# Performance work log

Hardware: AMD Instinct MI355X
Metric: run time of the kernel (lower is better)

The kernel has to match this reference:

```python
import jax, jax.numpy as jnp
import numpy as np

N = 50000
E_G = 600000
E_K = 500000
IN_FEATS = 64
H = 128
C = 2
# calculate_theta2(d=2): Bernstein polynomial coefficients (ascending powers)
THETAS_G = [[3.0, -3.0, 0.75], [0.0, 3.0, -1.5], [0.0, 0.0, 0.75]]
THETAS_K = [[1.0, 1.0, 1.0]] * 3


def _xavier(key, shape):
    fan_in, fan_out = shape[1], shape[0]
    lim = float(np.sqrt(6.0 / (fan_in + fan_out)))
    return jax.random.uniform(key, shape, jnp.float32, -lim, lim)


def setup_inputs() -> dict:
    key = jax.random.key(0)
    ks = jax.random.split(key, 32)
    inp = {
        "x": jax.random.normal(ks[0], (N, IN_FEATS), jnp.float32),
        "src_g": jax.random.randint(ks[1], (E_G,), 0, N, jnp.int32),
        "dst_g": jax.random.randint(ks[2], (E_G,), 0, N, jnp.int32),
        "src_k": jax.random.randint(ks[3], (E_K,), 0, N, jnp.int32),
        "dst_k": jax.random.randint(ks[4], (E_K,), 0, N, jnp.int32),
        # input MLP
        "W1": _xavier(ks[5], (H, IN_FEATS)), "b1": jnp.zeros((H,), jnp.float32),
        "W2": _xavier(ks[6], (H, H)), "b2": jnp.zeros((H,), jnp.float32),
        # 3 PolyConvs on main graph: learnable_diag [3,3,H], linear [3,H,H]+bias
        "diag_g": jax.random.uniform(ks[7], (3, 3, H), jnp.float32),
        "Wc_g": jnp.stack([_xavier(ks[8 + i], (H, H)) for i in range(3)]),
        "bc_g": jnp.zeros((3, H), jnp.float32),
        # 3 PolyConvs on knn graph
        "diag_k": jax.random.uniform(ks[11], (3, 3, H), jnp.float32),
        "Wc_k": jnp.stack([_xavier(ks[12 + i], (H, H)) for i in range(3)]),
        "bc_k": jnp.zeros((3, H), jnp.float32),
        # fusion linears (3H -> H)
        "W3": _xavier(ks[15], (H, 3 * H)), "b3": jnp.zeros((H,), jnp.float32),
        "Wk": _xavier(ks[16], (H, 3 * H)), "bk": jnp.zeros((H,), jnp.float32),
        # ComponentAttention: Linear(H,H)+Tanh+Linear(H,1,no bias)
        "Wa1": _xavier(ks[17], (H, H)), "ba1": jnp.zeros((H,), jnp.float32),
        "Wa2": _xavier(ks[18], (1, H)),
        # classifier
        "W4": _xavier(ks[19], (C, H)), "b4": jnp.zeros((C,), jnp.float32),
    }
    return inp


def _dinvsqrt(dst, n):
    deg = jax.ops.segment_sum(jnp.ones(dst.shape, jnp.float32), dst, num_segments=n)
    return jnp.clip(deg, 1.0, None) ** -0.5  # [N]


def _poly_conv(feat, src, dst, dinv, theta, diag, W, b, n):
    # h = linear(theta[0]*feat * diag[0]); then k-1 Laplacian hops
    h = jnp.dot((theta[0] * feat) * diag[0], W.T) + b
    for k in range(1, len(theta)):
        m = feat * dinv  # [N,H]
        agg = jax.ops.segment_sum(m[src], dst, num_segments=n)  # SpMM
        feat = feat - (agg * dinv) * diag[k]
        h = h + theta[k] * feat
    return h


def reference(x, src_g, dst_g, src_k, dst_k, W1, b1, W2, b2, diag_g, Wc_g, bc_g,
              diag_k, Wc_k, bc_k, W3, b3, Wk, bk, Wa1, ba1, Wa2, W4, b4):
    dinv_g = _dinvsqrt(dst_g, N)[:, None]
    dinv_k = _dinvsqrt(dst_k, N)[:, None]

    h = jax.nn.relu(jnp.dot(x, W1.T) + b1)
    h = jax.nn.relu(jnp.dot(h, W2.T) + b2)

    h_o = jnp.concatenate(
        [_poly_conv(h, src_g, dst_g, dinv_g, THETAS_G[i], diag_g[i], Wc_g[i], bc_g[i], N)
         for i in range(3)], axis=-1)
    h_o = jax.nn.relu(jnp.dot(h_o, W3.T) + b3)

    h_knn = jnp.concatenate(
        [_poly_conv(h, src_k, dst_k, dinv_k, THETAS_K[i], diag_k[i], Wc_k[i], bc_k[i], N)
         for i in range(3)], axis=-1)
    h_knn = jax.nn.relu(jnp.dot(h_knn, Wk.T) + bk)

    z = jnp.stack([h_o, h_knn], axis=1)  # [N,2,H]
    w = jnp.dot(jnp.tanh(jnp.dot(z, Wa1.T) + ba1), Wa2.T)  # [N,2,1]
    beta = jax.nn.softmax(w.mean(axis=0), axis=0)  # [2,1]
    emb = (beta[None] * z).sum(axis=1)  # [N,H]

    logits = jnp.dot(emb, W4.T) + b4
    return (logits, emb)
```

## Files before the change

### kernel.cpp

```cpp
#include <hip/hip_runtime.h>
#include <math.h>

#define NN 50000
#define EG 600000
#define EK 500000
#define H 128
#define INF 64
#define NB 196

#define GRID 512

struct Theta9 { float t[9]; };

__device__ __forceinline__ float f4_at(const float4& v, int i) {
  return i == 0 ? v.x : i == 1 ? v.y : i == 2 ? v.z : v.w;
}
__device__ __forceinline__ void fma4(float4& a, float s, const float4& w) {
  a.x += s * w.x; a.y += s * w.y; a.z += s * w.z; a.w += s * w.w;
}
__device__ __forceinline__ float4 relu4(float4 a) {
  a.x = fmaxf(a.x, 0.f); a.y = fmaxf(a.y, 0.f);
  a.z = fmaxf(a.z, 0.f); a.w = fmaxf(a.w, 0.f);
  return a;
}
__device__ __forceinline__ float fast_tanh(float x) {
  float a = fabsf(x);
  float t = __expf(-2.f * a);
  float r = (1.f - t) * __builtin_amdgcn_rcpf(1.f + t);
  return copysignf(r, x);
}
__device__ __forceinline__ float dot_tanh4(const float4& w2, const float4& a) {
  return w2.x * fast_tanh(a.x) + w2.y * fast_tanh(a.y) +
         w2.z * fast_tanh(a.z) + w2.w * fast_tanh(a.w);
}


__global__ __launch_bounds__(256) void k_hist(const int* __restrict__ dg,
    const int* __restrict__ dk, int* __restrict__ cg, int* __restrict__ ck) {
  __shared__ int h[512];
  int t = threadIdx.x;
  h[t] = 0; h[t + 256] = 0;
  __syncthreads();
  for (int e = blockIdx.x * 256 + t; e < EG; e += gridDim.x * 256) {
    atomicAdd(&h[dg[e] >> 8], 1);
    if (e < EK) atomicAdd(&h[256 + (dk[e] >> 8)], 1);
  }
  __syncthreads();
  if (t < NB) {
    if (h[t]) atomicAdd(&cg[t], h[t]);
    if (h[256 + t]) atomicAdd(&ck[t], h[256 + t]);
  }
}

__global__ __launch_bounds__(256) void k_bscan(const int* __restrict__ cg,
    const int* __restrict__ ck, int* __restrict__ bg, int* __restrict__ bk,
    int* __restrict__ curg, int* __restrict__ curk,
    int* __restrict__ rpg, int* __restrict__ rpk) {
  __shared__ int sg[256], sk[256];
  int t = threadIdx.x;
  int vg = (t < NB) ? cg[t] : 0;
  int vk = (t < NB) ? ck[t] : 0;
  sg[t] = vg; sk[t] = vk;
  __syncthreads();
  for (int d = 1; d < 256; d <<= 1) {
    int ug = (t >= d) ? sg[t - d] : 0;
    int uk = (t >= d) ? sk[t - d] : 0;
    __syncthreads();
    sg[t] += ug; sk[t] += uk;
    __syncthreads();
  }
  int eg = sg[t] - vg, ek = sk[t] - vk;
  if (t < NB) {
    bg[t] = eg; bk[t] = ek;
    curg[t] = eg; curk[t] = ek;
  }
  if (t == NB - 1) {
    bg[NB] = eg + vg; bk[NB] = ek + vk;
    rpg[NN] = eg + vg; rpk[NN] = ek + vk;
  }
}

template<int E>
__global__ __launch_bounds__(256) void k_part(const int* __restrict__ src,
    const int* __restrict__ dst, int* __restrict__ gcur, int2* __restrict__ ebuf) {
  __shared__ int hist[NB], lbase[NB], cur[NB];
  int t = threadIdx.x;
  int CH = (E + gridDim.x - 1) / gridDim.x;
  int b0 = blockIdx.x * CH;
  int b1 = min(E, b0 + CH);
  if (t < NB) hist[t] = 0;
  __syncthreads();
  for (int e = b0 + t; e < b1; e += 256) atomicAdd(&hist[dst[e] >> 8], 1);
  __syncthreads();
  if (t < NB && hist[t]) lbase[t] = atomicAdd(&gcur[t], hist[t]);
  __syncthreads();
  if (t < NB) cur[t] = 0;
  __syncthreads();
  for (int e = b0 + t; e < b1; e += 256) {
    int d = dst[e];
    int b = d >> 8;
    int r = atomicAdd(&cur[b], 1);
    ebuf[lbase[b] + r] = make_int2(src[e], d);
  }
}

__global__ __launch_bounds__(256) void k_bcsr(const int2* __restrict__ ebuf,
    const int* __restrict__ bbase, int* __restrict__ rp, int* __restrict__ adj,
    float* __restrict__ dinv) {
  __shared__ int hist[256], incl[256], cur[256];
  int t = threadIdx.x, b = blockIdx.x;
  int beg = bbase[b], end = bbase[b + 1];
  int node0 = b << 8;
  int nvalid = min(256, NN - node0);
  hist[t] = 0;
  __syncthreads();
  for (int i = beg + t; i < end; i += 256) atomicAdd(&hist[ebuf[i].y - node0], 1);
  __syncthreads();
  incl[t] = hist[t];
  __syncthreads();
  for (int d = 1; d < 256; d <<= 1) {
    int u = (t >= d) ? incl[t - d] : 0;
    __syncthreads();
    incl[t] += u;
    __syncthreads();
  }
  int excl = incl[t] - hist[t];
  if (t < nvalid) {
    rp[node0 + t] = beg + excl;
    int dg = hist[t]; if (dg < 1) dg = 1;
    dinv[node0 + t] = rsqrtf((float)dg);
  }
  cur[t] = 0;
  incl[t] = excl;
  __syncthreads();
  for (int i = beg + t; i < end; i += 256) {
    int2 ed = ebuf[i];
    int d = ed.y - node0;
    int r = atomicAdd(&cur[d], 1);
    adj[beg + incl[d] + r] = ed.x;
  }
}

__global__ __launch_bounds__(256) void k_transpose(const float* __restrict__ A,
    float* __restrict__ At, int R, int C) {
  int i = blockIdx.x * 256 + threadIdx.x;
  if (i < R * C) {
    int r = i / C, c = i % C;
    At[c * R + r] = A[i];
  }
}

__global__ __launch_bounds__(256) void k_genmat(const float* __restrict__ diag,
    const float* __restrict__ Wc, const float* __restrict__ W3, Theta9 th,
    float* __restrict__ A, float* __restrict__ B, float* __restrict__ C) {
  int id = blockIdx.x * 256 + threadIdx.x;
  int k = id >> 7, j = id & 127;
  float a = 0.f, b = 0.f, c = 0.f;
  for (int i = 0; i < 3; i++) {
    float t0 = th.t[i * 3 + 0], t1 = th.t[i * 3 + 1], t2 = th.t[i * 3 + 2];
    float d0 = diag[(i * 3 + 0) * H + k];
    float d1 = diag[(i * 3 + 1) * H + k];
    float d2 = diag[(i * 3 + 2) * H + k];
    float ci = t0 * d0;
    float alpha = t1 + t2;
    float beta  = -((t1 + t2) * d1 + t2 * d2);
    float gamma = t2 * d1 * d2;
    float w3kj = W3[j * 384 + i * H + k];
    if (ci != 0.f) {
      const float* Wi = Wc + i * H * H;
      float g = 0.f;
      for (int m = 0; m < H; m++)
        g += Wi[m * H + k] * W3[j * 384 + i * H + m];
      a += ci * g;
    }
    a += alpha * w3kj;
    b += beta * w3kj;
    c += gamma * w3kj;
  }
  A[id] = a; B[id] = b; C[id] = c;
}

__global__ __launch_bounds__(256) void k_genbias(const float* __restrict__ bc,
    const float* __restrict__ W3, const float* __restrict__ b3, float* __restrict__ bias) {
  int j = threadIdx.x;
  float s = b3[j];
  for (int i = 0; i < 3; i++)
    for (int m = 0; m < H; m++)
      s += bc[i * H + m] * W3[j * 384 + i * H + m];
  bias[j] = s;
}

__device__ __forceinline__ void accum_tile(const float* __restrict__ X, int t,
    const float* __restrict__ wlds, int lane, float4* a) {
  int n0 = t * 6;
  const float* x0 = X + (size_t)n0 * H;
  if (n0 + 6 <= NN) {
    for (int k = 0; k < H; k += 4) {
      float4 xv[6];
#pragma unroll
      for (int i = 0; i < 6; i++)
        xv[i] = *(const float4*)(x0 + (size_t)i * H + k);
#pragma unroll
      for (int kk = 0; kk < 4; kk++) {
        float4 w = *(const float4*)(wlds + (k + kk) * H + lane * 4);
#pragma unroll
        for (int i = 0; i < 6; i++) fma4(a[i], f4_at(xv[i], kk), w);
      }
    }
  } else {
    int nv = NN - n0;
    for (int k = 0; k < H; k += 4) {
      float4 xv[6];
#pragma unroll
      for (int i = 0; i < 6; i++)
        xv[i] = (i < nv) ? *(const float4*)(x0 + (size_t)i * H + k)
                         : make_float4(0.f, 0.f, 0.f, 0.f);
#pragma unroll
      for (int kk = 0; kk < 4; kk++) {
        float4 w = *(const float4*)(wlds + (k + kk) * H + lane * 4);
#pragma unroll
        for (int i = 0; i < 6; i++) fma4(a[i], f4_at(xv[i], kk), w);
      }
    }
  }
}

__device__ __forceinline__ void write_tile(float* __restrict__ Y, int t, int lane,
    float4* a) {
  int n0 = t * 6;
  int nv = min(6, NN - n0);
  float* y = Y + (size_t)n0 * H + lane * 4;
#pragma unroll
  for (int i = 0; i < 6; i++) {
    if (i < nv) *(float4*)(y + (size_t)i * H) = relu4(a[i]);
  }
}

template<int K>
__global__ __launch_bounds__(512) void k_gemm(const float* __restrict__ X,
    const float* __restrict__ Wt, const float* __restrict__ bias,
    float* __restrict__ Y) {
  __shared__ float wlds[K * H];
#pragma unroll
  for (int i = 0; i < K * H / 2048; i++) {
    int idx = (threadIdx.x + i * 512) * 4;
    *(float4*)(wlds + idx) = *(const float4*)(Wt + idx);
  }
  __syncthreads();
  const int lane = threadIdx.x & 31;
  float4 bb = *(const float4*)(bias + lane * 4);
  const int NT = (NN + 5) / 6;
  const int g0 = (threadIdx.x >> 5) * gridDim.x + blockIdx.x;
  const int stride = gridDim.x * 16;
  for (int t = g0; t < NT; t += stride) {
    int n0 = t * 6;
    const float* x0 = X + (size_t)n0 * K;
    float4 a[6];
#pragma unroll
    for (int i = 0; i < 6; i++) a[i] = bb;
    if (n0 + 6 <= NN) {
      for (int k = 0; k < K; k += 4) {
        float4 xv[6];
#pragma unroll
        for (int i = 0; i < 6; i++)
          xv[i] = *(const float4*)(x0 + (size_t)i * K + k);
#pragma unroll
        for (int kk = 0; kk < 4; kk++) {
          float4 w = *(const float4*)(wlds + (k + kk) * H + lane * 4);
#pragma unroll
          for (int i = 0; i < 6; i++) fma4(a[i], f4_at(xv[i], kk), w);
        }
      }
    } else {
      int nv = NN - n0;
      for (int k = 0; k < K; k += 4) {
        float4 xv[6];
#pragma unroll
        for (int i = 0; i < 6; i++)
          xv[i] = (i < nv) ? *(const float4*)(x0 + (size_t)i * K + k)
                           : make_float4(0.f, 0.f, 0.f, 0.f);
#pragma unroll
        for (int kk = 0; kk < 4; kk++) {
          float4 w = *(const float4*)(wlds + (k + kk) * H + lane * 4);
#pragma unroll
          for (int i = 0; i < 6; i++) fma4(a[i], f4_at(xv[i], kk), w);
        }
      }
    }
    write_tile(Y, t, lane, a);
  }
}

__global__ __launch_bounds__(512) void k_lin3f(const float* __restrict__ X0,
    const float* __restrict__ X1, const float* __restrict__ X2,
    const float* __restrict__ A, const float* __restrict__ B,
    const float* __restrict__ C, const float* __restrict__ bias,
    float* __restrict__ Y) {
  __shared__ float wlds[H * H];
  const int lane = threadIdx.x & 31;
  const int g0 = (threadIdx.x >> 5) * gridDim.x + blockIdx.x;
  const int NG = gridDim.x * 16;
  const int NT = (NN + 5) / 6;
  const int t0 = g0, t1 = g0 + NG;
  float4 bb = *(const float4*)(bias + lane * 4);
  float4 a0[6], a1[6];
#pragma unroll
  for (int i = 0; i < 6; i++) { a0[i] = bb; a1[i] = bb; }

#define PHASE(W, X)                                                      \
  {                                                                      \
    __syncthreads();                                                     \
    _Pragma("unroll")                                                    \
    for (int i = 0; i < 8; i++) {                                        \
      int idx = (threadIdx.x + i * 512) * 4;                             \
      *(float4*)(wlds + idx) = *(const float4*)((W) + idx);              \
    }                                                                    \
    __syncthreads();                                                     \
    accum_tile((X), t0, wlds, lane, a0);                                 \
    if (t1 < NT) accum_tile((X), t1, wlds, lane, a1);                    \
  }

  PHASE(A, X0)
  PHASE(B, X1)
  PHASE(C, X2)
#undef PHASE

  write_tile(Y, t0, lane, a0);
  if (t1 < NT) write_tile(Y, t1, lane, a1);
}

__global__ __launch_bounds__(512) void k_attn(const float* __restrict__ Ho,
    const float* __restrict__ Hk, const float* __restrict__ Wa1t,
    const float* __restrict__ ba1, const float* __restrict__ Wa2,
    float* __restrict__ sums) {
  __shared__ float wlds[H * H];
#pragma unroll
  for (int i = 0; i < 8; i++) {
    int idx = (threadIdx.x + i * 512) * 4;
    *(float4*)(wlds + idx) = *(const float4*)(Wa1t + idx);
  }
  __syncthreads();
  const int lane = threadIdx.x & 31;
  float4 bb = *(const float4*)(ba1 + lane * 4);
  float4 w2 = *(const float4*)(Wa2 + lane * 4);
  const int g0 = (threadIdx.x >> 5) * gridDim.x + blockIdx.x;
  const int stride = gridDim.x * 16;
  float po = 0.f, pk = 0.f;
  for (int t = g0; t < NN / 4; t += stride) {
    int n0 = t * 4;
    const float* ho = Ho + (size_t)n0 * H;
    const float* hk = Hk + (size_t)n0 * H;
    float4 ao[4], ak[4];
#pragma unroll
    for (int i = 0; i < 4; i++) { ao[i] = bb; ak[i] = bb; }
    for (int k = 0; k < H; k += 4) {
      float4 xo[4], xk[4];
#pragma unroll
      for (int i = 0; i < 4; i++) {
        xo[i] = *(const float4*)(ho + (size_t)i * H + k);
        xk[i] = *(const float4*)(hk + (size_t)i * H + k);
      }
#pragma unroll
      for (int kk = 0; kk < 4; kk++) {
        float4 w = *(const float4*)(wlds + (k + kk) * H + lane * 4);
#pragma unroll
        for (int i = 0; i < 4; i++) {
          fma4(ao[i], f4_at(xo[i], kk), w);
          fma4(ak[i], f4_at(xk[i], kk), w);
        }
      }
    }
#pragma unroll
    for (int i = 0; i < 4; i++) {
      po += dot_tanh4(w2, ao[i]);
      pk += dot_tanh4(w2, ak[i]);
    }
  }
  for (int d = 32; d > 0; d >>= 1) {
    po += __shfl_down(po, d, 64);
    pk += __shfl_down(pk, d, 64);
  }
  __syncthreads();
  int wv = threadIdx.x >> 6;
  if ((threadIdx.x & 63) == 0) { wlds[wv] = po; wlds[8 + wv] = pk; }
  __syncthreads();
  if (threadIdx.x == 0) {
    float so = 0.f, sk = 0.f;
    for (int i = 0; i < 8; i++) { so += wlds[i]; sk += wlds[8 + i]; }
    atomicAdd(&sums[0], so);
    atomicAdd(&sums[1], sk);
  }
}

__global__ __launch_bounds__(256) void k_spmm(const float* __restrict__ X,
    const float* __restrict__ dinv, const int* __restrict__ rp,
    const int* __restrict__ adj, float* __restrict__ Y) {
  int g = blockIdx.x * blockDim.x + threadIdx.x;
  int n = g >> 5, lane = g & 31;
  if (n >= NN) return;
  float4 acc = make_float4(0.f, 0.f, 0.f, 0.f);
  int beg = rp[n], end = rp[n + 1];
  const float* Xl = X + lane * 4;
  int e = beg;
  for (; e + 4 <= end; e += 4) {
    int s0 = adj[e], s1 = adj[e + 1], s2 = adj[e + 2], s3 = adj[e + 3];
    float d0 = dinv[s0], d1 = dinv[s1], d2 = dinv[s2], d3 = dinv[s3];
    float4 v0 = *(const float4*)(Xl + (size_t)s0 * H);
    float4 v1 = *(const float4*)(Xl + (size_t)s1 * H);
    float4 v2 = *(const float4*)(Xl + (size_t)s2 * H);
    float4 v3 = *(const float4*)(Xl + (size_t)s3 * H);
    fma4(acc, d0, v0);
    fma4(acc, d1, v1);
    fma4(acc, d2, v2);
    fma4(acc, d3, v3);
  }
  for (; e < end; e++) {
    int s = adj[e];
    fma4(acc, dinv[s], *(const float4*)(Xl + (size_t)s * H));
  }
  float dn = dinv[n];
  acc.x *= dn; acc.y *= dn; acc.z *= dn; acc.w *= dn;
  *(float4*)(Y + (size_t)n * H + lane * 4) = acc;
}

__global__ __launch_bounds__(256) void k_final(const float* __restrict__ Ho,
    const float* __restrict__ Hk, const float* __restrict__ sums,
    const float* __restrict__ W4, const float* __restrict__ b4,
    float* __restrict__ out) {
  int g = blockIdx.x * blockDim.x + threadIdx.x;
  int n = g >> 5, lane = g & 31;
  if (n >= NN) return;
  float mo = sums[0] * (1.f / NN);
  float mk = sums[1] * (1.f / NN);
  float mx = fmaxf(mo, mk);
  float eo = __expf(mo - mx), ek = __expf(mk - mx);
  float inv = 1.f / (eo + ek);
  float bo = eo * inv, bk2 = ek * inv;
  float4 ho = *(const float4*)(Ho + (size_t)n * H + lane * 4);
  float4 hk = *(const float4*)(Hk + (size_t)n * H + lane * 4);
  float4 emb;
  emb.x = bo * ho.x + bk2 * hk.x;
  emb.y = bo * ho.y + bk2 * hk.y;
  emb.z = bo * ho.z + bk2 * hk.z;
  emb.w = bo * ho.w + bk2 * hk.w;
  *(float4*)(out + 2 * NN + (size_t)n * H + lane * 4) = emb;
  float4 w0 = *(const float4*)(W4 + lane * 4);
  float4 w1 = *(const float4*)(W4 + H + lane * 4);
  float p0 = emb.x * w0.x + emb.y * w0.y + emb.z * w0.z + emb.w * w0.w;
  float p1 = emb.x * w1.x + emb.y * w1.y + emb.z * w1.z + emb.w * w1.w;
  for (int d = 16; d > 0; d >>= 1) {
    p0 += __shfl_down(p0, d, 32);
    p1 += __shfl_down(p1, d, 32);
  }
  if (lane == 0) {
    out[n * 2 + 0] = p0 + b4[0];
    out[n * 2 + 1] = p1 + b4[1];
  }
}

extern "C" void kernel_launch(void* const* d_in, const int* in_sizes, int n_in,
                              void* d_out, int out_size, void* d_ws, size_t ws_size,
                              hipStream_t stream) {
  const float* x      = (const float*)d_in[0];
  const int*   src_g  = (const int*)d_in[1];
  const int*   dst_g  = (const int*)d_in[2];
  const int*   src_k  = (const int*)d_in[3];
  const int*   dst_k  = (const int*)d_in[4];
  const float* W1     = (const float*)d_in[5];
  const float* b1     = (const float*)d_in[6];
  const float* W2     = (const float*)d_in[7];
  const float* b2     = (const float*)d_in[8];
  const float* diag_g = (const float*)d_in[9];
  const float* Wc_g   = (const float*)d_in[10];
  const float* bc_g   = (const float*)d_in[11];
  const float* diag_k = (const float*)d_in[12];
  const float* Wc_k   = (const float*)d_in[13];
  const float* bc_k   = (const float*)d_in[14];
  const float* W3     = (const float*)d_in[15];
  const float* b3     = (const float*)d_in[16];
  const float* Wk     = (const float*)d_in[17];
  const float* bk     = (const float*)d_in[18];
  const float* Wa1    = (const float*)d_in[19];
  const float* ba1    = (const float*)d_in[20];
  const float* Wa2    = (const float*)d_in[21];
  const float* W4     = (const float*)d_in[22];
  const float* b4     = (const float*)d_in[23];
  float* out = (float*)d_out;

  char* base = (char*)d_ws;
  size_t off = 0;
  auto alloc = [&](size_t bytes) -> char* {
    char* r = base + off;
    off = (off + bytes + 255) & ~(size_t)255;
    return r;
  };
  int* bcnt_g = (int*)alloc(256 * 4);
  int* bcnt_k = (int*)alloc(256 * 4);
  float* sums = (float*)alloc(256);
  size_t zero_bytes = off;

  int* bbase_g = (int*)alloc((NB + 1) * 4);
  int* bbase_k = (int*)alloc((NB + 1) * 4);
  int* bcur_g  = (int*)alloc(NB * 4);
  int* bcur_k  = (int*)alloc(NB * 4);
  int* rp_g    = (int*)alloc((NN + 1) * 4);
  int* rp_k    = (int*)alloc((NN + 1) * 4);
  int2* ebuf_g = (int2*)alloc((size_t)EG * 8);
  int2* ebuf_k = (int2*)alloc((size_t)EK * 8);
  int* adj_g   = (int*)alloc(EG * 4);
  int* adj_k   = (int*)alloc(EK * 4);
  float* dinv_g = (float*)alloc(NN * 4);
  float* dinv_k = (float*)alloc(NN * 4);
  float* Wt1  = (float*)alloc(INF * H * 4);
  float* Wt2  = (float*)alloc(H * H * 4);
  float* Wa1t = (float*)alloc(H * H * 4);
  float* Ag = (float*)alloc(H * H * 4);
  float* Bg = (float*)alloc(H * H * 4);
  float* Cg = (float*)alloc(H * H * 4);
  float* biasg = (float*)alloc(H * 4);
  float* Ak = (float*)alloc(H * H * 4);
  float* Bk = (float*)alloc(H * H * 4);
  float* Ck = (float*)alloc(H * H * 4);
  float* biask = (float*)alloc(H * 4);
  float* B0 = (float*)alloc((size_t)NN * H * 4);
  float* B1 = (float*)alloc((size_t)NN * H * 4);
  float* B2 = (float*)alloc((size_t)NN * H * 4);
  float* B3 = (float*)alloc((size_t)NN * H * 4);
  float* B4 = (float*)alloc((size_t)NN * H * 4);
  (void)ws_size; (void)in_sizes; (void)n_in; (void)out_size;

  hipMemsetAsync(d_ws, 0, zero_bytes, stream);

  const int GB = NN * 32 / 256;

  k_hist<<<512, 256, 0, stream>>>(dst_g, dst_k, bcnt_g, bcnt_k);
  k_bscan<<<1, 256, 0, stream>>>(bcnt_g, bcnt_k, bbase_g, bbase_k,
                                 bcur_g, bcur_k, rp_g, rp_k);
  k_part<EG><<<512, 256, 0, stream>>>(src_g, dst_g, bcur_g, ebuf_g);
  k_part<EK><<<512, 256, 0, stream>>>(src_k, dst_k, bcur_k, ebuf_k);
  k_bcsr<<<NB, 256, 0, stream>>>(ebuf_g, bbase_g, rp_g, adj_g, dinv_g);
  k_bcsr<<<NB, 256, 0, stream>>>(ebuf_k, bbase_k, rp_k, adj_k, dinv_k);

  k_transpose<<<(H * INF + 255) / 256, 256, 0, stream>>>(W1, Wt1, H, INF);
  k_transpose<<<(H * H + 255) / 256, 256, 0, stream>>>(W2, Wt2, H, H);
  k_transpose<<<(H * H + 255) / 256, 256, 0, stream>>>(Wa1, Wa1t, H, H);
  Theta9 thG = {{3.f, -3.f, 0.75f, 0.f, 3.f, -1.5f, 0.f, 0.f, 0.75f}};
  Theta9 thK = {{1.f, 1.f, 1.f, 1.f, 1.f, 1.f, 1.f, 1.f, 1.f}};
  k_genmat<<<64, 256, 0, stream>>>(diag_g, Wc_g, W3, thG, Ag, Bg, Cg);
  k_genmat<<<64, 256, 0, stream>>>(diag_k, Wc_k, Wk, thK, Ak, Bk, Ck);
  k_genbias<<<1, 128, 0, stream>>>(bc_g, W3, b3, biasg);
  k_genbias<<<1, 128, 0, stream>>>(bc_k, Wk, bk, biask);

  k_gemm<INF><<<GRID, 512, 0, stream>>>(x, Wt1, b1, B0);
  k_gemm<H><<<GRID, 512, 0, stream>>>(B0, Wt2, b2, B1);

  k_spmm<<<GB, 256, 0, stream>>>(B1, dinv_g, rp_g, adj_g, B2);
  k_spmm<<<GB, 256, 0, stream>>>(B2, dinv_g, rp_g, adj_g, B3);
  k_lin3f<<<GRID, 512, 0, stream>>>(B1, B2, B3, Ag, Bg, Cg, biasg, B0);

  k_spmm<<<GB, 256, 0, stream>>>(B1, dinv_k, rp_k, adj_k, B2);
  k_spmm<<<GB, 256, 0, stream>>>(B2, dinv_k, rp_k, adj_k, B3);
  k_lin3f<<<GRID, 512, 0, stream>>>(B1, B2, B3, Ak, Bk, Ck, biask, B4);

  k_attn<<<GRID, 512, 0, stream>>>(B0, B4, Wa1t, ba1, Wa2, sums);
  k_final<<<GB, 256, 0, stream>>>(B0, B4, sums, W4, b4, out);
}
```

Baseline: 704.0 us.

## Prefetch GEMM inputs, unroll SpMM gather by 8, retile first MLP layer

accum_tile now double-buffers the X row loads, fetching the next k-slice while the current one is used in FMAs. The SpMM gather loop is unrolled by 8 so more independent loads are in flight per wavefront. The first linear layer (K=64) becomes a dedicated kernel that processes 4 rows per warp over a 1024-block grid with no grid-stride loop, and the K=128 layer reuses the shared accum_tile. These changes aim to hide memory latency in gather- and load-bound loops, at the cost of more registers per thread and possibly lower occupancy.

```diff
diff --git a/kernel.cpp b/kernel.cpp
--- a/kernel.cpp
+++ b/kernel.cpp
@@ -33,7 +33,6 @@
   return w2.x * fast_tanh(a.x) + w2.y * fast_tanh(a.y) +
          w2.z * fast_tanh(a.z) + w2.w * fast_tanh(a.w);
 }
-
 
 __global__ __launch_bounds__(256) void k_hist(const int* __restrict__ dg,
     const int* __restrict__ dk, int* __restrict__ cg, int* __restrict__ ck) {
@@ -195,17 +194,22 @@
   int n0 = t * 6;
   const float* x0 = X + (size_t)n0 * H;
   if (n0 + 6 <= NN) {
+    float4 xa[6], xb[6];
+#pragma unroll
+    for (int i = 0; i < 6; i++) xa[i] = *(const float4*)(x0 + (size_t)i * H);
     for (int k = 0; k < H; k += 4) {
-      float4 xv[6];
+      int kn = (k + 4 < H) ? (k + 4) : k;
 #pragma unroll
       for (int i = 0; i < 6; i++)
-        xv[i] = *(const float4*)(x0 + (size_t)i * H + k);
+        xb[i] = *(const float4*)(x0 + (size_t)i * H + kn);
 #pragma unroll
       for (int kk = 0; kk < 4; kk++) {
         float4 w = *(const float4*)(wlds + (k + kk) * H + lane * 4);
 #pragma unroll
-        for (int i = 0; i < 6; i++) fma4(a[i], f4_at(xv[i], kk), w);
+        for (int i = 0; i < 6; i++) fma4(a[i], f4_at(xa[i], kk), w);
       }
+#pragma unroll
+      for (int i = 0; i < 6; i++) xa[i] = xb[i];
     }
   } else {
     int nv = NN - n0;
@@ -236,13 +240,66 @@
   }
 }
 
-template<int K>
-__global__ __launch_bounds__(512) void k_gemm(const float* __restrict__ X,
+__global__ __launch_bounds__(512) void k_gemm64(const float* __restrict__ X,
     const float* __restrict__ Wt, const float* __restrict__ bias,
     float* __restrict__ Y) {
-  __shared__ float wlds[K * H];
-#pragma unroll
-  for (int i = 0; i < K * H / 2048; i++) {
+  __shared__ float wlds[INF * H];
+#pragma unroll
+  for (int i = 0; i < 4; i++) {
+    int idx = (threadIdx.x + i * 512) * 4;
+    *(float4*)(wlds + idx) = *(const float4*)(Wt + idx);
+  }
+  __syncthreads();
+  const int lane = threadIdx.x & 31;
+  const int g = (threadIdx.x >> 5) * gridDim.x + blockIdx.x;
+  const int n0 = g * 4;
+  if (n0 >= NN) return;
+  const int nv = min(4, NN - n0);
+  float4 bb = *(const float4*)(bias + lane * 4);
+  float4 a[4];
+#pragma unroll
+  for (int i = 0; i < 4; i++) a[i] = bb;
+  const float* x0 = X + (size_t)n0 * INF;
+  if (nv == 4) {
+    for (int k = 0; k < INF; k += 4) {
+      float4 xv[4];
+#pragma unroll
+      for (int i = 0; i < 4; i++)
+        xv[i] = *(const float4*)(x0 + (size_t)i * INF + k);
+#pragma unroll
+      for (int kk = 0; kk < 4; kk++) {
+        float4 w = *(const float4*)(wlds + (k + kk) * H + lane * 4);
+#pragma unroll
+        for (int i = 0; i < 4; i++) fma4(a[i], f4_at(xv[i], kk), w);
+      }
+    }
+  } else {
+    for (int k = 0; k < INF; k += 4) {
+      float4 xv[4];
+#pragma unroll
+      for (int i = 0; i < 4; i++)
+        xv[i] = (i < nv) ? *(const float4*)(x0 + (size_t)i * INF + k)
+                         : make_float4(0.f, 0.f, 0.f, 0.f);
+#pragma unroll
+      for (int kk = 0; kk < 4; kk++) {
+        float4 w = *(const float4*)(wlds + (k + kk) * H + lane * 4);
+#pragma unroll
+        for (int i = 0; i < 4; i++) fma4(a[i], f4_at(xv[i], kk), w);
+      }
+    }
+  }
+  float* y = Y + (size_t)n0 * H + lane * 4;
+#pragma unroll
+  for (int i = 0; i < 4; i++)
+    if (i < nv) *(float4*)(y + (size_t)i * H) = relu4(a[i]);
+}
+
+__global__ __launch_bounds__(512) void k_gemmH(const float* __restrict__ X,
+    const float* __restrict__ Wt, const float* __restrict__ bias,
+    float* __restrict__ Y) {
+  __shared__ float wlds[H * H];
+#pragma unroll
+  for (int i = 0; i < 8; i++) {
     int idx = (threadIdx.x + i * 512) * 4;
     *(float4*)(wlds + idx) = *(const float4*)(Wt + idx);
   }
@@ -253,40 +310,10 @@
   const int g0 = (threadIdx.x >> 5) * gridDim.x + blockIdx.x;
   const int stride = gridDim.x * 16;
   for (int t = g0; t < NT; t += stride) {
-    int n0 = t * 6;
-    const float* x0 = X + (size_t)n0 * K;
     float4 a[6];
 #pragma unroll
     for (int i = 0; i < 6; i++) a[i] = bb;
-    if (n0 + 6 <= NN) {
-      for (int k = 0; k < K; k += 4) {
-        float4 xv[6];
-#pragma unroll
-        for (int i = 0; i < 6; i++)
-          xv[i] = *(const float4*)(x0 + (size_t)i * K + k);
-#pragma unroll
-        for (int kk = 0; kk < 4; kk++) {
-          float4 w = *(const float4*)(wlds + (k + kk) * H + lane * 4);
-#pragma unroll
-          for (int i = 0; i < 6; i++) fma4(a[i], f4_at(xv[i], kk), w);
-        }
-      }
-    } else {
-      int nv = NN - n0;
-      for (int k = 0; k < K; k += 4) {
-        float4 xv[6];
-#pragma unroll
-        for (int i = 0; i < 6; i++)
-          xv[i] = (i < nv) ? *(const float4*)(x0 + (size_t)i * K + k)
-                           : make_float4(0.f, 0.f, 0.f, 0.f);
-#pragma unroll
-        for (int kk = 0; kk < 4; kk++) {
-          float4 w = *(const float4*)(wlds + (k + kk) * H + lane * 4);
-#pragma unroll
-          for (int i = 0; i < 6; i++) fma4(a[i], f4_at(xv[i], kk), w);
-        }
-      }
-    }
+    accum_tile(X, t, wlds, lane, a);
     write_tile(Y, t, lane, a);
   }
 }
@@ -402,6 +429,19 @@
   int beg = rp[n], end = rp[n + 1];
   const float* Xl = X + lane * 4;
   int e = beg;
+  for (; e + 8 <= end; e += 8) {
+    int s[8];
+#pragma unroll
+    for (int j = 0; j < 8; j++) s[j] = adj[e + j];
+    float d[8];
+#pragma unroll
+    for (int j = 0; j < 8; j++) d[j] = dinv[s[j]];
+    float4 v[8];
+#pragma unroll
+    for (int j = 0; j < 8; j++) v[j] = *(const float4*)(Xl + (size_t)s[j] * H);
+#pragma unroll
+    for (int j = 0; j < 8; j++) fma4(acc, d[j], v[j]);
+  }
   for (; e + 4 <= end; e += 4) {
     int s0 = adj[e], s1 = adj[e + 1], s2 = adj[e + 2], s3 = adj[e + 3];
     float d0 = dinv[s0], d1 = dinv[s1], d2 = dinv[s2], d3 = dinv[s3];
@@ -551,8 +591,8 @@
   k_genbias<<<1, 128, 0, stream>>>(bc_g, W3, b3, biasg);
   k_genbias<<<1, 128, 0, stream>>>(bc_k, Wk, bk, biask);
 
-  k_gemm<INF><<<GRID, 512, 0, stream>>>(x, Wt1, b1, B0);
-  k_gemm<H><<<GRID, 512, 0, stream>>>(B0, Wt2, b2, B1);
+  k_gemm64<<<1024, 512, 0, stream>>>(x, Wt1, b1, B0);
+  k_gemmH<<<GRID, 512, 0, stream>>>(B0, Wt2, b2, B1);
 
   k_spmm<<<GB, 256, 0, stream>>>(B1, dinv_g, rp_g, adj_g, B2);
   k_spmm<<<GB, 256, 0, stream>>>(B2, dinv_g, rp_g, adj_g, B3);
```

After: 684.8 us. 1.03x faster.
